# Optimization experiments

Measured on AMD Instinct MI355X. Metric: run time of the kernel, lower is better.

## Reference

```python
import jax, jax.numpy as jnp
import numpy as np

B, NS, NN = 1024, 1, 64
F = 128            # feat_dim = edge_dim = time_dim = pos_dim
DM = 4 * F         # model_dim = 512
H, DK = 2, 256     # n_head, d_k = d_v = model_dim // n_head
LN_EPS = 1e-5


def setup_inputs() -> dict:
    key = jax.random.key(0)
    ks = jax.random.split(key, 20)
    s = 0.02
    inp = {
        'src':   jax.random.normal(ks[0], (B, NS, F), jnp.float32),
        'src_t': jax.random.normal(ks[1], (B, NS, F), jnp.float32),
        'src_p': jax.random.normal(ks[2], (B, NS, F), jnp.float32),
        'seq':   jax.random.normal(ks[3], (B, NN, F), jnp.float32),
        'seq_t': jax.random.normal(ks[4], (B, NN, F), jnp.float32),
        'seq_e': jax.random.normal(ks[5], (B, NN, F), jnp.float32),
        'seq_p': jax.random.normal(ks[6], (B, NN, F), jnp.float32),
        'mask':  jax.random.randint(ks[7], (B, NS, NN), 0, 2).astype(bool),
        # MapBasedMultiHeadAttention params
        'wq': jax.random.normal(ks[8], (H * DK, DM), jnp.float32) * s,
        'wk': jax.random.normal(ks[9], (H * DK, DM), jnp.float32) * s,
        'wv': jax.random.normal(ks[10], (H * DK, DM), jnp.float32) * s,
        'wm': jax.random.normal(ks[11], (2 * DK,), jnp.float32) * s,   # weight_map: Linear(2*d_k, 1, bias=False)
        'fc_w': jax.random.normal(ks[12], (DM, H * DK), jnp.float32) * s,
        'fc_b': jnp.zeros((DM,), jnp.float32),
        'ln_g': jnp.ones((DM,), jnp.float32),
        'ln_b': jnp.zeros((DM,), jnp.float32),
        # MergeLayer(model_dim, feat_dim, feat_dim, feat_dim)
        'm1_w': jax.random.normal(ks[13], (F, DM + F), jnp.float32) * s,
        'm1_b': jnp.zeros((F,), jnp.float32),
        'm2_w': jax.random.normal(ks[14], (F, F), jnp.float32) * s,
        'm2_b': jnp.zeros((F,), jnp.float32),
    }
    return inp


def reference(src, src_t, src_p, seq, seq_t, seq_e, seq_p, mask,
              wq, wk, wv, wm, fc_w, fc_b, ln_g, ln_b, m1_w, m1_b, m2_w, m2_b):
    b, ns, f = src.shape
    nn = seq.shape[1]
    src_e = jnp.zeros((b, ns, f), src.dtype)  # edge feats of sources are zero
    q = jnp.concatenate([src, src_e, src_t, src_p], axis=-1)   # [B,NS,DM]
    k = jnp.concatenate([seq, seq_e, seq_t, seq_p], axis=-1)   # [B,NN,DM]

    # per-head projections: weight [H*DK, DM] -> [H, DK, DM]
    qh = jnp.einsum('bsd,hed->bshe', q, wq.reshape(H, DK, DM))  # [B,NS,H,DK]
    kh = jnp.einsum('bnd,hed->bnhe', k, wk.reshape(H, DK, DM))  # [B,NN,H,DK]
    vh = jnp.einsum('bnd,hed->bnhe', k, wv.reshape(H, DK, DM))  # [B,NN,H,DK]

    # weight_map(Linear over concat([q,k])) == q @ wm[:DK] + k @ wm[DK:]
    score_q = jnp.einsum('bshe,e->bhs', qh, wm[:DK])            # [B,H,NS]
    score_k = jnp.einsum('bnhe,e->bhn', kh, wm[DK:])            # [B,H,NN]
    attn = score_q[..., None] + score_k[:, :, None, :]          # [B,H,NS,NN]
    attn = jnp.where(mask[:, None, :, :], jnp.float32(-1e10), attn)
    attn = jax.nn.softmax(attn, axis=-1)

    out = jnp.einsum('bhsn,bnhe->bshe', attn, vh).reshape(b, ns, H * DK)
    out = jnp.einsum('bsd,ed->bse', out, fc_w) + fc_b           # fc
    out = jnp.where(out >= 0, out, 0.2 * out)                   # LeakyReLU(0.2)
    out = out + q                                               # residual
    mu = out.mean(axis=-1, keepdims=True)
    var = out.var(axis=-1, keepdims=True)
    out = (out - mu) / jnp.sqrt(var + LN_EPS) * ln_g + ln_b     # LayerNorm

    # MergeLayer (non_linear=True)
    x = jnp.concatenate([out, src], axis=-1)                    # [B,NS,DM+F]
    hdn = jax.nn.relu(jnp.einsum('bsd,ed->bse', x, m1_w) + m1_b)
    z = jnp.einsum('bsd,ed->bse', hdn, m2_w) + m2_b             # [B,NS,F]

    # attn in original layout: [n_head*B, len_q, len_k]
    attn_flat = attn.transpose(1, 0, 2, 3).reshape(H * b, ns, nn)
    return (z, attn_flat)
```

## Files before the change

### kernel.cpp

```cpp
#include <hip/hip_runtime.h>
#include <hip/hip_bf16.h>
#include <stdint.h>

#define B_   1024
#define NN_  64
#define F_   128
#define DM_  512
#define DK_  256

typedef unsigned short u16;
using f32x4  = __attribute__((ext_vector_type(4))) float;
using bf16x8 = __attribute__((ext_vector_type(8))) short;

__device__ __forceinline__ uint32_t f2bf(float x) {
  uint32_t u = __builtin_bit_cast(uint32_t, x);
  return (u + 0x7fffu + ((u >> 16) & 1u)) >> 16;
}
__device__ __forceinline__ float bf2f(uint32_t us) {
  return __builtin_bit_cast(float, us << 16);
}
__device__ __forceinline__ void split_pack(float x, float y, uint32_t& hp, uint32_t& lp) {
  uint32_t hx = f2bf(x), hy = f2bf(y);
  uint32_t lx = f2bf(x - bf2f(hx)), ly = f2bf(y - bf2f(hy));
  hp = hx | (hy << 16);
  lp = lx | (ly << 16);
}
__device__ __forceinline__ void split1(float x, u16& h, u16& l) {
  uint32_t hx = f2bf(x);
  h = (u16)hx;
  l = (u16)f2bf(x - bf2f(hx));
}
template <int CTRL>
__device__ __forceinline__ float dppadd(float x) {
  int r = __builtin_amdgcn_mov_dpp(__builtin_bit_cast(int, x), CTRL, 0xF, 0xF, true);
  return x + __builtin_bit_cast(float, r);
}
__device__ __forceinline__ float red16(float p) {
  p = dppadd<0xB1>(p);
  p = dppadd<0x4E>(p);
  p = dppadd<0x114>(p);
  p = dppadd<0x118>(p);
  return p;
}

__global__ __launch_bounds__(256) void k_prep(
    const float* __restrict__ wv, const float* __restrict__ fc_w,
    const float* __restrict__ m1_w, const float* __restrict__ m2_w,
    const float* __restrict__ wk, const float* __restrict__ wm,
    u16* __restrict__ fc_hi, u16* __restrict__ fc_lo,
    u16* __restrict__ wvT_hi, u16* __restrict__ wvT_lo,
    u16* __restrict__ m1_hi, u16* __restrict__ m1_lo,
    u16* __restrict__ m2_hi, u16* __restrict__ m2_lo,
    float* __restrict__ wkc) {
  __shared__ float tile[32][33];
  int tid = threadIdx.x;
  int bx = blockIdx.x;

  if (bx >= 256) {
    int t = bx - 256;
    int h = t >> 3, dc = t & 7;
    int w = tid >> 6, l = tid & 63;
    int d = dc * 64 + l;
    const float* base = wk + (size_t)(h * DK_ + w * 64) * DM_ + d;
    float sacc[8] = {0.f, 0.f, 0.f, 0.f, 0.f, 0.f, 0.f, 0.f};
    #pragma unroll
    for (int e = 0; e < 64; ++e)
      sacc[e & 7] += base[e * DM_] * wm[DK_ + w * 64 + e];
    float s = ((sacc[0] + sacc[1]) + (sacc[2] + sacc[3])) +
              ((sacc[4] + sacc[5]) + (sacc[6] + sacc[7]));
    float* part = &tile[0][0];
    part[w * 64 + l] = s;
    __syncthreads();
    if (w == 0)
      wkc[h * DM_ + d] = part[l] + part[64 + l] + part[128 + l] + part[192 + l];
    return;
  }

  int gtid = bx * 256 + tid;
  int nthr = 256 * 256;
  for (int i = gtid; i < DM_ * DM_; i += nthr) split1(fc_w[i], fc_hi[i], fc_lo[i]);
  for (int i = gtid; i < F_ * (DM_ + F_); i += nthr) split1(m1_w[i], m1_hi[i], m1_lo[i]);
  for (int i = gtid; i < F_ * F_; i += nthr) split1(m2_w[i], m2_hi[i], m2_lo[i]);

  int e0 = (bx >> 4) * 32, d0 = (bx & 15) * 32;
  int rr = tid >> 3, c4 = (tid & 7) * 4;
  float4 v = *(const float4*)(wv + (e0 + rr) * DM_ + d0 + c4);
  tile[rr][c4] = v.x; tile[rr][c4 + 1] = v.y;
  tile[rr][c4 + 2] = v.z; tile[rr][c4 + 3] = v.w;
  __syncthreads();
  int dr = tid >> 3, ec = (tid & 7) * 4;
  #pragma unroll
  for (int q = 0; q < 4; ++q) {
    int idx = (d0 + dr) * DM_ + e0 + ec + q;
    split1(tile[ec + q][dr], wvT_hi[idx], wvT_lo[idx]);
  }
}

__device__ __forceinline__ f32x4 mfma_tile_split(
    const u16* __restrict__ Ahi, const u16* __restrict__ Alo, int lda,
    const u16* __restrict__ Bhi, const u16* __restrict__ Blo, int ldb, int K) {
  int l = threadIdx.x & 63;
  int r = l & 15, g = l >> 4;
  int offA = r * lda + g * 8;
  int offB = r * ldb + g * 8;
  f32x4 acc = {0.f, 0.f, 0.f, 0.f};
  for (int k = 0; k < K; k += 32) {
    bf16x8 ah = *(const bf16x8*)(Ahi + offA + k);
    bf16x8 al = *(const bf16x8*)(Alo + offA + k);
    bf16x8 bh = *(const bf16x8*)(Bhi + offB + k);
    bf16x8 bl = *(const bf16x8*)(Blo + offB + k);
    acc = __builtin_amdgcn_mfma_f32_16x16x32_bf16(ah, bh, acc, 0, 0, 0);
    acc = __builtin_amdgcn_mfma_f32_16x16x32_bf16(ah, bl, acc, 0, 0, 0);
    acc = __builtin_amdgcn_mfma_f32_16x16x32_bf16(al, bh, acc, 0, 0, 0);
  }
  return acc;
}

__global__ __launch_bounds__(256) void k_wcomb(
    const u16* __restrict__ fc_hi, const u16* __restrict__ fc_lo,
    const u16* __restrict__ wvT_hi, const u16* __restrict__ wvT_lo,
    u16* __restrict__ wc_hi, u16* __restrict__ wc_lo) {
  int wid = threadIdx.x >> 6;
  int n0g = blockIdx.y * 32;
  int h = n0g >> 9, d0 = n0g & 511;
  int m0 = blockIdx.x * 32 + (wid >> 1) * 16;
  int nb = d0 + (wid & 1) * 16;
  f32x4 acc = mfma_tile_split(fc_hi + m0 * DM_ + h * DK_,
                              fc_lo + m0 * DM_ + h * DK_, DM_,
                              wvT_hi + nb * DM_ + h * DK_,
                              wvT_lo + nb * DM_ + h * DK_, DM_, DK_);
  int l = threadIdx.x & 63, r = l & 15, g = l >> 4;
  #pragma unroll
  for (int i = 0; i < 4; ++i) {
    int m = m0 + g * 4 + i;
    int idx = m * 1024 + n0g + (wid & 1) * 16 + r;
    split1(acc[i], wc_hi[idx], wc_lo[idx]);
  }
}

__global__ __launch_bounds__(256) void k_attn(
    const float* __restrict__ seq, const float* __restrict__ seq_e,
    const float* __restrict__ seq_t, const float* __restrict__ seq_p,
    const int* __restrict__ mask, const float* __restrict__ wkc,
    float* __restrict__ attn_out,
    uint32_t* __restrict__ kbar_hi, uint32_t* __restrict__ kbar_lo) {
  __shared__ float pbuf[4][2][8][4];
  __shared__ float els[2][64];
  __shared__ float Zs[2];
  int tid = threadIdx.x, b = blockIdx.x;
  int w = tid >> 6, l = tid & 63;
  int c16 = l & 15;

  const float* arr = (w == 0 ? seq : (w == 1 ? seq_e : (w == 2 ? seq_t : seq_p)));
  const float* base = arr + (size_t)b * 8192 + 2 * l;
  float c00 = wkc[w * 128 + 2 * l],       c01 = wkc[w * 128 + 2 * l + 1];
  float c10 = wkc[512 + w * 128 + 2 * l], c11 = wkc[512 + w * 128 + 2 * l + 1];
  float kb00 = 0.f, kb01 = 0.f, kb10 = 0.f, kb11 = 0.f;

  for (int bt = 0; bt < 8; ++bt) {
    float2 v[8];
    #pragma unroll
    for (int u = 0; u < 8; ++u)
      v[u] = *(const float2*)(base + (size_t)(bt * 8 + u) * 128);
    #pragma unroll
    for (int u = 0; u < 8; ++u) {
      float p0 = v[u].x * c00 + v[u].y * c01;
      float p1 = v[u].x * c10 + v[u].y * c11;
      p0 = red16(p0);
      p1 = red16(p1);
      if (c16 == 12) {
        pbuf[w][0][u][l >> 4] = p0;
        pbuf[w][1][u][l >> 4] = p1;
      }
    }
    __syncthreads();
    if (tid < 16) {
      int u = tid & 7, h = tid >> 3;
      float s = 0.f;
      #pragma unroll
      for (int ww = 0; ww < 4; ++ww)
        #pragma unroll
        for (int g = 0; g < 4; ++g) s += pbuf[ww][h][u][g];
      int row = bt * 8 + u;
      els[h][row] = mask[b * 64 + row] ? 0.f : expf(s);
    }
    __syncthreads();
    #pragma unroll
    for (int u = 0; u < 8; ++u) {
      int row = bt * 8 + u;
      float e0 = els[0][row], e1 = els[1][row];
      kb00 += e0 * v[u].x; kb01 += e0 * v[u].y;
      kb10 += e1 * v[u].x; kb11 += e1 * v[u].y;
    }
  }

  if (tid < 128) {
    int h = tid >> 6, row = tid & 63;
    float e = els[h][row];
    float z = e;
    #pragma unroll
    for (int off = 32; off; off >>= 1) z += __shfl_xor(z, off);
    attn_out[(h * B_ + b) * 64 + row] = e / z;
    if (row == 0) Zs[h] = z;
  }
  __syncthreads();
  float r0 = 1.f / Zs[0], r1 = 1.f / Zs[1];
  uint32_t hp, lp;
  int idx = b * 512 + tid;
  split_pack(kb00 * r0, kb01 * r0, hp, lp);
  kbar_hi[idx] = hp; kbar_lo[idx] = lp;
  split_pack(kb10 * r1, kb11 * r1, hp, lp);
  kbar_hi[idx + 256] = hp; kbar_lo[idx + 256] = lp;
}

__global__ __launch_bounds__(256) void k_fc(
    const u16* __restrict__ kb_hi, const u16* __restrict__ kb_lo,
    const u16* __restrict__ wc_hi, const u16* __restrict__ wc_lo,
    const float* __restrict__ fc_b,
    const float* __restrict__ src, const float* __restrict__ src_t,
    const float* __restrict__ src_p, float* __restrict__ fco) {
  int tid = threadIdx.x;
  int wid = tid >> 6, l = tid & 63;
  int r = l & 15, g = l >> 4;
  int m0 = blockIdx.x * 32 + (wid >> 1) * 16;
  int n0 = blockIdx.y * 64 + (wid & 1) * 32;
  int offA  = (m0 + r) * 1024 + g * 8;
  int offB0 = (n0 + r) * 1024 + g * 8;
  int offB1 = offB0 + 16 * 1024;
  f32x4 acc0 = {0.f, 0.f, 0.f, 0.f}, acc1 = {0.f, 0.f, 0.f, 0.f};
  #pragma unroll 4
  for (int k = 0; k < 1024; k += 32) {
    bf16x8 ah  = *(const bf16x8*)(kb_hi + offA + k);
    bf16x8 al  = *(const bf16x8*)(kb_lo + offA + k);
    bf16x8 b0h = *(const bf16x8*)(wc_hi + offB0 + k);
    bf16x8 b0l = *(const bf16x8*)(wc_lo + offB0 + k);
    bf16x8 b1h = *(const bf16x8*)(wc_hi + offB1 + k);
    bf16x8 b1l = *(const bf16x8*)(wc_lo + offB1 + k);
    acc0 = __builtin_amdgcn_mfma_f32_16x16x32_bf16(ah, b0h, acc0, 0, 0, 0);
    acc0 = __builtin_amdgcn_mfma_f32_16x16x32_bf16(ah, b0l, acc0, 0, 0, 0);
    acc0 = __builtin_amdgcn_mfma_f32_16x16x32_bf16(al, b0h, acc0, 0, 0, 0);
    acc1 = __builtin_amdgcn_mfma_f32_16x16x32_bf16(ah, b1h, acc1, 0, 0, 0);
    acc1 = __builtin_amdgcn_mfma_f32_16x16x32_bf16(ah, b1l, acc1, 0, 0, 0);
    acc1 = __builtin_amdgcn_mfma_f32_16x16x32_bf16(al, b1h, acc1, 0, 0, 0);
  }
  #pragma unroll
  for (int f = 0; f < 2; ++f) {
    int col = n0 + f * 16 + r;
    int part = col >> 7, fc2 = col & 127;
    float bias = fc_b[col];
    const float* qsrc = (part == 0 ? src : (part == 2 ? src_t : src_p));
    #pragma unroll
    for (int i = 0; i < 4; ++i) {
      int m = m0 + g * 4 + i;
      float c = (f == 0 ? acc0[i] : acc1[i]) + bias;
      c = (c >= 0.f) ? c : 0.2f * c;
      float qv = (part == 1) ? 0.f : qsrc[m * 128 + fc2];
      fco[m * 512 + col] = c + qv;
    }
  }
}

__global__ __launch_bounds__(512) void k_m12(
    const float* __restrict__ fco, const float* __restrict__ ln_g,
    const float* __restrict__ ln_b, const float* __restrict__ src,
    const u16* __restrict__ m1_hi, const u16* __restrict__ m1_lo,
    const float* __restrict__ m1_b,
    const u16* __restrict__ m2_hi, const u16* __restrict__ m2_lo,
    const float* __restrict__ m2_b, float* __restrict__ z) {
  __shared__ u16 xh[16][648], xl[16][648];
  __shared__ u16 hh[16][136], hl[16][136];
  int tid = threadIdx.x;
  int m0 = blockIdx.x * 16;

  {
    int row = tid >> 5, l32 = tid & 31;
    int grow = m0 + row;
    float v[16];
    float s = 0.f, s2 = 0.f;
    #pragma unroll
    for (int q = 0; q < 16; ++q) {
      v[q] = fco[grow * 512 + q * 32 + l32];
      s += v[q]; s2 += v[q] * v[q];
    }
    #pragma unroll
    for (int off = 16; off; off >>= 1) {
      s += __shfl_xor(s, off, 32);
      s2 += __shfl_xor(s2, off, 32);
    }
    float mu = s * (1.f / 512.f);
    float var = s2 * (1.f / 512.f) - mu * mu;
    float rstd = rsqrtf(var + 1e-5f);
    #pragma unroll
    for (int q = 0; q < 16; ++q) {
      int col = q * 32 + l32;
      float o = (v[q] - mu) * rstd * ln_g[col] + ln_b[col];
      split1(o, xh[row][col], xl[row][col]);
    }
    #pragma unroll
    for (int q2 = 0; q2 < 4; ++q2) {
      int c = q2 * 32 + l32;
      split1(src[grow * 128 + c], xh[row][512 + c], xl[row][512 + c]);
    }
  }
  __syncthreads();

  int wid = tid >> 6, l = tid & 63;
  int r = l & 15, g = l >> 4;
  int nb = wid * 16;
  {
    f32x4 acc = mfma_tile_split(&xh[0][0], &xl[0][0], 648,
                                m1_hi + nb * 640, m1_lo + nb * 640, 640, 640);
    int col = nb + r;
    float bias = m1_b[col];
    #pragma unroll
    for (int ii = 0; ii < 4; ++ii) {
      int row = g * 4 + ii;
      float o = fmaxf(acc[ii] + bias, 0.f);
      split1(o, hh[row][col], hl[row][col]);
    }
  }
  __syncthreads();
  {
    f32x4 acc = mfma_tile_split(&hh[0][0], &hl[0][0], 136,
                                m2_hi + nb * 128, m2_lo + nb * 128, 128, 128);
    int col = nb + r;
    float bias = m2_b[col];
    #pragma unroll
    for (int ii = 0; ii < 4; ++ii) {
      int row = g * 4 + ii;
      z[(m0 + row) * 128 + col] = acc[ii] + bias;
    }
  }
}

extern "C" void kernel_launch(void* const* d_in, const int* in_sizes, int n_in,
                              void* d_out, int out_size, void* d_ws, size_t ws_size,
                              hipStream_t stream) {
  (void)in_sizes; (void)n_in; (void)out_size; (void)ws_size;
  const float* src   = (const float*)d_in[0];
  const float* src_t = (const float*)d_in[1];
  const float* src_p = (const float*)d_in[2];
  const float* seq   = (const float*)d_in[3];
  const float* seq_t = (const float*)d_in[4];
  const float* seq_e = (const float*)d_in[5];
  const float* seq_p = (const float*)d_in[6];
  const int*   mask  = (const int*)d_in[7];
  const float* wk   = (const float*)d_in[9];
  const float* wv   = (const float*)d_in[10];
  const float* wm   = (const float*)d_in[11];
  const float* fc_w = (const float*)d_in[12];
  const float* fc_b = (const float*)d_in[13];
  const float* ln_g = (const float*)d_in[14];
  const float* ln_b = (const float*)d_in[15];
  const float* m1_w = (const float*)d_in[16];
  const float* m1_b = (const float*)d_in[17];
  const float* m2_w = (const float*)d_in[18];
  const float* m2_b = (const float*)d_in[19];

  float* z_out    = (float*)d_out;
  float* attn_out = z_out + B_ * F_;

  char* ws = (char*)d_ws;
  float* wkc     = (float*)(ws + 0);
  u16* fc_hi     = (u16*)(ws + 4096);
  u16* fc_lo     = (u16*)(ws + 528384);
  u16* m1_hi     = (u16*)(ws + 1052672);
  u16* m1_lo     = (u16*)(ws + 1216512);
  u16* m2_hi     = (u16*)(ws + 1380352);
  u16* m2_lo     = (u16*)(ws + 1413120);
  u16* wvT_hi    = (u16*)(ws + 1445888);
  u16* wvT_lo    = (u16*)(ws + 1970176);
  u16* wc_hi     = (u16*)(ws + 2494464);
  u16* wc_lo     = (u16*)(ws + 3543040);
  uint32_t* kbhi = (uint32_t*)(ws + 4591616);
  uint32_t* kblo = (uint32_t*)(ws + 6688768);
  float* fco     = (float*)(ws + 8785920);

  hipLaunchKernelGGL(k_prep, dim3(272), dim3(256), 0, stream,
                     wv, fc_w, m1_w, m2_w, wk, wm,
                     fc_hi, fc_lo, wvT_hi, wvT_lo,
                     m1_hi, m1_lo, m2_hi, m2_lo, wkc);
  hipLaunchKernelGGL(k_attn, dim3(1024), dim3(256), 0, stream,
                     seq, seq_e, seq_t, seq_p, mask, wkc,
                     attn_out, kbhi, kblo);
  hipLaunchKernelGGL(k_wcomb, dim3(16, 32), dim3(256), 0, stream,
                     fc_hi, fc_lo, wvT_hi, wvT_lo, wc_hi, wc_lo);
  hipLaunchKernelGGL(k_fc, dim3(32, 8), dim3(256), 0, stream,
                     (const u16*)kbhi, (const u16*)kblo, wc_hi, wc_lo, fc_b,
                     src, src_t, src_p, fco);
  hipLaunchKernelGGL(k_m12, dim3(64), dim3(512), 0, stream,
                     fco, ln_g, ln_b, src,
                     m1_hi, m1_lo, m1_b, m2_hi, m2_lo, m2_b, z_out);
}
```

Before: 80.71 us.

## Split attention kernel over neighbor halves with atomic partial sums and normalize pass

The per-batch attention kernel is split into two blocks per batch row, each handling 32 of the 64 neighbors. Each block writes its unnormalized exp scores to a buffer and atomically adds its partial weighted sums into a zeroed workspace. A new normalization kernel then computes the softmax denominators, writes the attention output and packs the normalized sums into hi/lo bf16. This doubles the block count to raise parallelism, at the cost of a memset, 1024 float atomics per block, an extra launch and an extra round trip through global memory. P reuses the fco workspace region, which is safe only because the normalization kernel consumes P before k_fc writes fco.

Result: slower. 92.45 us (+14.5%).

```diff
diff --git a/kernel.cpp b/kernel.cpp
--- a/kernel.cpp
+++ b/kernel.cpp
@@ -138,26 +138,25 @@
   }
 }
 
-__global__ __launch_bounds__(256) void k_attn(
+__global__ __launch_bounds__(256) void k_attn_p(
     const float* __restrict__ seq, const float* __restrict__ seq_e,
     const float* __restrict__ seq_t, const float* __restrict__ seq_p,
     const int* __restrict__ mask, const float* __restrict__ wkc,
-    float* __restrict__ attn_out,
-    uint32_t* __restrict__ kbar_hi, uint32_t* __restrict__ kbar_lo) {
+    float* __restrict__ E, float* __restrict__ P) {
   __shared__ float pbuf[4][2][8][4];
-  __shared__ float els[2][64];
-  __shared__ float Zs[2];
-  int tid = threadIdx.x, b = blockIdx.x;
+  __shared__ float els[2][32];
+  int b = blockIdx.x, half = blockIdx.y;
+  int tid = threadIdx.x;
   int w = tid >> 6, l = tid & 63;
   int c16 = l & 15;
 
   const float* arr = (w == 0 ? seq : (w == 1 ? seq_e : (w == 2 ? seq_t : seq_p)));
-  const float* base = arr + (size_t)b * 8192 + 2 * l;
+  const float* base = arr + (size_t)b * 8192 + (size_t)half * 32 * 128 + 2 * l;
   float c00 = wkc[w * 128 + 2 * l],       c01 = wkc[w * 128 + 2 * l + 1];
   float c10 = wkc[512 + w * 128 + 2 * l], c11 = wkc[512 + w * 128 + 2 * l + 1];
   float kb00 = 0.f, kb01 = 0.f, kb10 = 0.f, kb11 = 0.f;
 
-  for (int bt = 0; bt < 8; ++bt) {
+  for (int bt = 0; bt < 4; ++bt) {
     float2 v[8];
     #pragma unroll
     for (int u = 0; u < 8; ++u)
@@ -181,22 +180,38 @@
       for (int ww = 0; ww < 4; ++ww)
         #pragma unroll
         for (int g = 0; g < 4; ++g) s += pbuf[ww][h][u][g];
-      int row = bt * 8 + u;
-      els[h][row] = mask[b * 64 + row] ? 0.f : expf(s);
+      int rl = bt * 8 + u;
+      int grow = half * 32 + rl;
+      float e = mask[b * 64 + grow] ? 0.f : expf(s);
+      els[h][rl] = e;
+      E[((size_t)b * 2 + h) * 64 + grow] = e;
     }
     __syncthreads();
     #pragma unroll
     for (int u = 0; u < 8; ++u) {
-      int row = bt * 8 + u;
-      float e0 = els[0][row], e1 = els[1][row];
+      int rl = bt * 8 + u;
+      float e0 = els[0][rl], e1 = els[1][rl];
       kb00 += e0 * v[u].x; kb01 += e0 * v[u].y;
       kb10 += e1 * v[u].x; kb11 += e1 * v[u].y;
     }
   }
 
+  float* Pb = P + (size_t)b * 1024;
+  atomicAdd(Pb + 2 * tid,       kb00);
+  atomicAdd(Pb + 2 * tid + 1,   kb01);
+  atomicAdd(Pb + 512 + 2 * tid, kb10);
+  atomicAdd(Pb + 512 + 2 * tid + 1, kb11);
+}
+
+__global__ __launch_bounds__(256) void k_norm(
+    const float* __restrict__ E, const float* __restrict__ P,
+    float* __restrict__ attn_out,
+    uint32_t* __restrict__ kbar_hi, uint32_t* __restrict__ kbar_lo) {
+  __shared__ float Zs[2];
+  int b = blockIdx.x, tid = threadIdx.x;
   if (tid < 128) {
     int h = tid >> 6, row = tid & 63;
-    float e = els[h][row];
+    float e = E[((size_t)b * 2 + h) * 64 + row];
     float z = e;
     #pragma unroll
     for (int off = 32; off; off >>= 1) z += __shfl_xor(z, off);
@@ -205,12 +220,14 @@
   }
   __syncthreads();
   float r0 = 1.f / Zs[0], r1 = 1.f / Zs[1];
+  const float2* Pb = (const float2*)(P + (size_t)b * 1024);
+  float2 q0 = Pb[tid];
+  float2 q1 = Pb[256 + tid];
   uint32_t hp, lp;
-  int idx = b * 512 + tid;
-  split_pack(kb00 * r0, kb01 * r0, hp, lp);
-  kbar_hi[idx] = hp; kbar_lo[idx] = lp;
-  split_pack(kb10 * r1, kb11 * r1, hp, lp);
-  kbar_hi[idx + 256] = hp; kbar_lo[idx + 256] = lp;
+  split_pack(q0.x * r0, q0.y * r0, hp, lp);
+  kbar_hi[b * 512 + tid] = hp; kbar_lo[b * 512 + tid] = lp;
+  split_pack(q1.x * r1, q1.y * r1, hp, lp);
+  kbar_hi[b * 512 + 256 + tid] = hp; kbar_lo[b * 512 + 256 + tid] = lp;
 }
 
 __global__ __launch_bounds__(256) void k_fc(
@@ -374,15 +391,19 @@
   u16* wc_lo     = (u16*)(ws + 3543040);
   uint32_t* kbhi = (uint32_t*)(ws + 4591616);
   uint32_t* kblo = (uint32_t*)(ws + 6688768);
+  float* P       = (float*)(ws + 8785920);
   float* fco     = (float*)(ws + 8785920);
+  float* E       = (float*)(ws + 12980224);
 
   hipLaunchKernelGGL(k_prep, dim3(272), dim3(256), 0, stream,
                      wv, fc_w, m1_w, m2_w, wk, wm,
                      fc_hi, fc_lo, wvT_hi, wvT_lo,
                      m1_hi, m1_lo, m2_hi, m2_lo, wkc);
-  hipLaunchKernelGGL(k_attn, dim3(1024), dim3(256), 0, stream,
-                     seq, seq_e, seq_t, seq_p, mask, wkc,
-                     attn_out, kbhi, kblo);
+  hipMemsetAsync(P, 0, 4194304, stream);
+  hipLaunchKernelGGL(k_attn_p, dim3(1024, 2), dim3(256), 0, stream,
+                     seq, seq_e, seq_t, seq_p, mask, wkc, E, P);
+  hipLaunchKernelGGL(k_norm, dim3(1024), dim3(256), 0, stream,
+                     E, P, attn_out, kbhi, kblo);
   hipLaunchKernelGGL(k_wcomb, dim3(16, 32), dim3(256), 0, stream,
                      fc_hi, fc_lo, wvT_hi, wvT_lo, wc_hi, wc_lo);
   hipLaunchKernelGGL(k_fc, dim3(32, 8), dim3(256), 0, stream,
```

## Restructure attention kernel into score pass then weighted-sum pass with one barrier

Applied to the files above, without the earlier changes.

The attention kernel now computes all 64 key scores in a single pass. Each lane loads float4 pairs and does an 8-wide dot product, then writes per-lane partials to a padded shared buffer, replacing the per-8-row DPP reductions and the two barriers per iteration. After one barrier, 128 threads sum the partials, apply the mask and exp, and normalize. A second pass then re-reads the seq rows (likely from cache) for the weighted sum. This trades the eight-step synchronised loop for a second read of the inputs and a larger shared-memory footprint.

Result: slower. 97.07 us (+20.3%).

```diff
diff --git a/kernel.cpp b/kernel.cpp
--- a/kernel.cpp
+++ b/kernel.cpp
@@ -29,18 +29,6 @@
   uint32_t hx = f2bf(x);
   h = (u16)hx;
   l = (u16)f2bf(x - bf2f(hx));
-}
-template <int CTRL>
-__device__ __forceinline__ float dppadd(float x) {
-  int r = __builtin_amdgcn_mov_dpp(__builtin_bit_cast(int, x), CTRL, 0xF, 0xF, true);
-  return x + __builtin_bit_cast(float, r);
-}
-__device__ __forceinline__ float red16(float p) {
-  p = dppadd<0xB1>(p);
-  p = dppadd<0x4E>(p);
-  p = dppadd<0x114>(p);
-  p = dppadd<0x118>(p);
-  return p;
 }
 
 __global__ __launch_bounds__(256) void k_prep(
@@ -138,65 +126,59 @@
   }
 }
 
-__global__ __launch_bounds__(256) void k_attn(
+__global__ __launch_bounds__(256) void k_attn3(
     const float* __restrict__ seq, const float* __restrict__ seq_e,
     const float* __restrict__ seq_t, const float* __restrict__ seq_p,
     const int* __restrict__ mask, const float* __restrict__ wkc,
     float* __restrict__ attn_out,
     uint32_t* __restrict__ kbar_hi, uint32_t* __restrict__ kbar_lo) {
-  __shared__ float pbuf[4][2][8][4];
+  __shared__ float pbuf[4][64][34];
   __shared__ float els[2][64];
   __shared__ float Zs[2];
   int tid = threadIdx.x, b = blockIdx.x;
   int w = tid >> 6, l = tid & 63;
-  int c16 = l & 15;
+  int rq = l >> 4, c16 = l & 15;
 
   const float* arr = (w == 0 ? seq : (w == 1 ? seq_e : (w == 2 ? seq_t : seq_p)));
-  const float* base = arr + (size_t)b * 8192 + 2 * l;
-  float c00 = wkc[w * 128 + 2 * l],       c01 = wkc[w * 128 + 2 * l + 1];
-  float c10 = wkc[512 + w * 128 + 2 * l], c11 = wkc[512 + w * 128 + 2 * l + 1];
-  float kb00 = 0.f, kb01 = 0.f, kb10 = 0.f, kb11 = 0.f;
-
-  for (int bt = 0; bt < 8; ++bt) {
-    float2 v[8];
-    #pragma unroll
-    for (int u = 0; u < 8; ++u)
-      v[u] = *(const float2*)(base + (size_t)(bt * 8 + u) * 128);
-    #pragma unroll
-    for (int u = 0; u < 8; ++u) {
-      float p0 = v[u].x * c00 + v[u].y * c01;
-      float p1 = v[u].x * c10 + v[u].y * c11;
-      p0 = red16(p0);
-      p1 = red16(p1);
-      if (c16 == 12) {
-        pbuf[w][0][u][l >> 4] = p0;
-        pbuf[w][1][u][l >> 4] = p1;
-      }
-    }
-    __syncthreads();
-    if (tid < 16) {
-      int u = tid & 7, h = tid >> 3;
-      float s = 0.f;
-      #pragma unroll
-      for (int ww = 0; ww < 4; ++ww)
-        #pragma unroll
-        for (int g = 0; g < 4; ++g) s += pbuf[ww][h][u][g];
-      int row = bt * 8 + u;
-      els[h][row] = mask[b * 64 + row] ? 0.f : expf(s);
-    }
-    __syncthreads();
-    #pragma unroll
-    for (int u = 0; u < 8; ++u) {
-      int row = bt * 8 + u;
-      float e0 = els[0][row], e1 = els[1][row];
-      kb00 += e0 * v[u].x; kb01 += e0 * v[u].y;
-      kb10 += e1 * v[u].x; kb11 += e1 * v[u].y;
-    }
-  }
+  const float* base = arr + (size_t)b * 8192 + 8 * c16;
+  float c0[8], c1[8];
+  #pragma unroll
+  for (int u = 0; u < 8; ++u) {
+    c0[u] = wkc[w * 128 + 8 * c16 + u];
+    c1[u] = wkc[512 + w * 128 + 8 * c16 + u];
+  }
+
+  #pragma unroll
+  for (int g = 0; g < 4; ++g) {
+    float4 va[4], vb[4];
+    #pragma unroll
+    for (int i = 0; i < 4; ++i) {
+      int row = (g * 4 + i) * 4 + rq;
+      va[i] = *(const float4*)(base + row * 128);
+      vb[i] = *(const float4*)(base + row * 128 + 4);
+    }
+    #pragma unroll
+    for (int i = 0; i < 4; ++i) {
+      int row = (g * 4 + i) * 4 + rq;
+      float p0 = va[i].x * c0[0] + va[i].y * c0[1] + va[i].z * c0[2] + va[i].w * c0[3]
+               + vb[i].x * c0[4] + vb[i].y * c0[5] + vb[i].z * c0[6] + vb[i].w * c0[7];
+      float p1 = va[i].x * c1[0] + va[i].y * c1[1] + va[i].z * c1[2] + va[i].w * c1[3]
+               + vb[i].x * c1[4] + vb[i].y * c1[5] + vb[i].z * c1[6] + vb[i].w * c1[7];
+      float2 t; t.x = p0; t.y = p1;
+      *(float2*)&pbuf[w][row][2 * c16] = t;
+    }
+  }
+  __syncthreads();
 
   if (tid < 128) {
     int h = tid >> 6, row = tid & 63;
-    float e = els[h][row];
+    float s = 0.f;
+    #pragma unroll
+    for (int ww = 0; ww < 4; ++ww)
+      #pragma unroll
+      for (int c = 0; c < 16; ++c) s += pbuf[ww][row][2 * c + h];
+    float e = mask[b * 64 + row] ? 0.f : expf(s);
+    els[h][row] = e;
     float z = e;
     #pragma unroll
     for (int off = 32; off; off >>= 1) z += __shfl_xor(z, off);
@@ -204,12 +186,29 @@
     if (row == 0) Zs[h] = z;
   }
   __syncthreads();
+
+  const float* colp = arr + (size_t)b * 8192 + 2 * l;
+  float a00 = 0.f, a01 = 0.f, a10 = 0.f, a11 = 0.f;
+  #pragma unroll
+  for (int jb = 0; jb < 64; jb += 8) {
+    float2 v[8];
+    #pragma unroll
+    for (int u = 0; u < 8; ++u)
+      v[u] = *(const float2*)(colp + (jb + u) * 128);
+    #pragma unroll
+    for (int u = 0; u < 8; ++u) {
+      int j = jb + u;
+      float t0 = els[0][j], t1 = els[1][j];
+      a00 += t0 * v[u].x; a01 += t0 * v[u].y;
+      a10 += t1 * v[u].x; a11 += t1 * v[u].y;
+    }
+  }
   float r0 = 1.f / Zs[0], r1 = 1.f / Zs[1];
   uint32_t hp, lp;
   int idx = b * 512 + tid;
-  split_pack(kb00 * r0, kb01 * r0, hp, lp);
+  split_pack(a00 * r0, a01 * r0, hp, lp);
   kbar_hi[idx] = hp; kbar_lo[idx] = lp;
-  split_pack(kb10 * r1, kb11 * r1, hp, lp);
+  split_pack(a10 * r1, a11 * r1, hp, lp);
   kbar_hi[idx + 256] = hp; kbar_lo[idx + 256] = lp;
 }
 
@@ -380,7 +379,7 @@
                      wv, fc_w, m1_w, m2_w, wk, wm,
                      fc_hi, fc_lo, wvT_hi, wvT_lo,
                      m1_hi, m1_lo, m2_hi, m2_lo, wkc);
-  hipLaunchKernelGGL(k_attn, dim3(1024), dim3(256), 0, stream,
+  hipLaunchKernelGGL(k_attn3, dim3(1024), dim3(256), 0, stream,
                      seq, seq_e, seq_t, seq_p, mask, wkc,
                      attn_out, kbhi, kblo);
   hipLaunchKernelGGL(k_wcomb, dim3(16, 32), dim3(256), 0, stream,
```
